# Optimization experiments

Measured on AMD Instinct MI355X. Metric: run time of the kernel, lower is better.

Reference implementation:

```python
import jax, jax.numpy as jnp
from jax import lax
import numpy as np

B, C, T, H, HEADS = 256, 16, 256, 128, 4
D = H // HEADS  # per-head graph-attention out_features = 32

def _ln(x, g, b, eps=1e-5):
    m = x.mean(-1, keepdims=True)
    v = ((x - m) ** 2).mean(-1, keepdims=True)
    return (x - m) / jnp.sqrt(v + eps) * g + b

def _gat(h_in, W, a_src, a_dst, adj):
    # GAT-style multi-head attention over channels with learnable additive adjacency mask
    n, c, _ = h_in.shape
    h = (h_in @ W).reshape(n, c, HEADS, D)
    es = jnp.einsum('nchd,hd->nch', h, a_src)
    ed = jnp.einsum('nchd,hd->nch', h, a_dst)
    e = jax.nn.leaky_relu(es[:, :, None, :] + ed[:, None, :, :], 0.2) + adj[None, :, :, None]
    a = jax.nn.softmax(e, axis=2)
    return jnp.einsum('nijh,njhd->nihd', a, h).reshape(n, c, HEADS * D)

def _lstm_dir(xseq, Wih, Whh, bih, bhh, reverse):
    b = xseq.shape[0]
    h0 = jnp.zeros((b, H), xseq.dtype)
    def step(carry, xt):
        hp, cp = carry
        g = xt @ Wih.T + hp @ Whh.T + bih + bhh
        i, f, gg, o = jnp.split(g, 4, axis=-1)  # torch gate order i,f,g,o
        cn = jax.nn.sigmoid(f) * cp + jax.nn.sigmoid(i) * jnp.tanh(gg)
        hn = jax.nn.sigmoid(o) * jnp.tanh(cn)
        return (hn, cn), hn
    _, hs = lax.scan(step, (h0, h0), jnp.swapaxes(xseq, 0, 1), reverse=reverse)
    return jnp.swapaxes(hs, 0, 1)

def setup_inputs():
    key = jax.random.key(0)
    ks = iter(jax.random.split(key, 80))
    def rn(shape, s=0.05):
        return jax.random.normal(next(ks), shape, jnp.float32) * s
    inp = {'x': jax.random.normal(next(ks), (B, C, T), jnp.float32)}
    inp.update(conv1_w=rn((32, 1, 7), 0.2), conv1_b=jnp.zeros((32,)), bn1_g=jnp.ones((32,)), bn1_b=jnp.zeros((32,)),
               conv2_w=rn((64, 32, 5), 0.1), conv2_b=jnp.zeros((64,)), bn2_g=jnp.ones((64,)), bn2_b=jnp.zeros((64,)))
    inp.update(g1_W=rn((64, H)), g1_asrc=rn((HEADS, D)), g1_adst=rn((HEADS, D)), g1_adj=rn((C, C)),
               n1_g=jnp.ones((H,)), n1_b=jnp.zeros((H,)),
               g2_W=rn((H, H)), g2_asrc=rn((HEADS, D)), g2_adst=rn((HEADS, D)), g2_adj=rn((C, C)),
               n2_g=jnp.ones((H,)), n2_b=jnp.zeros((H,)))
    for layer, din in ((0, H * C), (1, 2 * H)):
        for d in ('f', 'r'):
            inp['l%d%s_Wih' % (layer, d)] = rn((4 * H, din))
            inp['l%d%s_Whh' % (layer, d)] = rn((4 * H, H))
            inp['l%d%s_bih' % (layer, d)] = jnp.zeros((4 * H,))
            inp['l%d%s_bhh' % (layer, d)] = jnp.zeros((4 * H,))
    E = 2 * H
    inp.update(mha_wqkv=rn((3 * E, E)), mha_bqkv=jnp.zeros((3 * E,)), mha_wo=rn((E, E)), mha_bo=jnp.zeros((E,)),
               an_g=jnp.ones((E,)), an_b=jnp.zeros((E,)), pn_g=jnp.ones((2 * E,)), pn_b=jnp.zeros((2 * E,)),
               fc1_w=rn((H, 2 * E)), fc1_b=jnp.zeros((H,)), fc2_w=rn((1, H)), fc2_b=jnp.zeros((1,)))
    return inp

def reference(x, conv1_w, conv1_b, bn1_g, bn1_b, conv2_w, conv2_b, bn2_g, bn2_b,
              g1_W, g1_asrc, g1_adst, g1_adj, n1_g, n1_b,
              g2_W, g2_asrc, g2_adst, g2_adj, n2_g, n2_b,
              l0f_Wih, l0f_Whh, l0f_bih, l0f_bhh, l0r_Wih, l0r_Whh, l0r_bih, l0r_bhh,
              l1f_Wih, l1f_Whh, l1f_bih, l1f_bhh, l1r_Wih, l1r_Whh, l1r_bih, l1r_bhh,
              mha_wqkv, mha_bqkv, mha_wo, mha_bo, an_g, an_b, pn_g, pn_b,
              fc1_w, fc1_b, fc2_w, fc2_b):
    b, c, t = x.shape
    dn = ('NCH', 'OIH', 'NCH')
    # shared per-channel temporal conv: fold channels into batch (same math as the python loop)
    h = lax.conv_general_dilated(x.reshape(b * c, 1, t), conv1_w, (1,), [(3, 3)], dimension_numbers=dn) + conv1_b[None, :, None]
    h = jax.nn.gelu(h * bn1_g[None, :, None] + bn1_b[None, :, None], approximate=False)  # BN in eval mode
    h = lax.conv_general_dilated(h, conv2_w, (2,), [(2, 2)], dimension_numbers=dn) + conv2_b[None, :, None]
    h = jax.nn.gelu(h * bn2_g[None, :, None] + bn2_b[None, :, None], approximate=False)
    tc = h.shape[-1]  # 128
    # fold timesteps into batch: graph attention applied independently per t
    g = h.reshape(b, c, 64, tc).transpose(0, 3, 1, 2).reshape(b * tc, c, 64)
    g = _ln(jax.nn.relu(_gat(g, g1_W, g1_asrc, g1_adst, g1_adj)), n1_g, n1_b)
    g = _ln(jax.nn.relu(_gat(g, g2_W, g2_asrc, g2_adst, g2_adj)), n2_g, n2_b)
    seq = g.reshape(b, tc, c * H)  # (B, 128, 2048)
    o = jnp.concatenate([_lstm_dir(seq, l0f_Wih, l0f_Whh, l0f_bih, l0f_bhh, False),
                         _lstm_dir(seq, l0r_Wih, l0r_Whh, l0r_bih, l0r_bhh, True)], -1)
    o = jnp.concatenate([_lstm_dir(o, l1f_Wih, l1f_Whh, l1f_bih, l1f_bhh, False),
                         _lstm_dir(o, l1r_Wih, l1r_Whh, l1r_bih, l1r_bhh, True)], -1)
    e = o.shape[-1]
    hd = e // HEADS
    qkv = o @ mha_wqkv.T + mha_bqkv
    q, k, v = [z.reshape(b, tc, HEADS, hd).transpose(0, 2, 1, 3) for z in jnp.split(qkv, 3, axis=-1)]
    a = jax.nn.softmax(jnp.einsum('bhqd,bhkd->bhqk', q, k) * (hd ** -0.5), axis=-1)
    ao = jnp.einsum('bhqk,bhkd->bhqd', a, v).transpose(0, 2, 1, 3).reshape(b, tc, e) @ mha_wo.T + mha_bo
    att = _ln(ao + o, an_g, an_b)
    pooled = _ln(jnp.concatenate([att.mean(axis=1), att.max(axis=1)], axis=-1), pn_g, pn_b)
    return jax.nn.relu(pooled @ fc1_w.T + fc1_b) @ fc2_w.T + fc2_b
```

## Files before the change

### kernel.cpp

```cpp
#include <hip/hip_runtime.h>
#include <hip/hip_bf16.h>
#include <stdint.h>


typedef __attribute__((ext_vector_type(8))) short bh8;
typedef __attribute__((ext_vector_type(4))) float f32x4;

__device__ __forceinline__ float bfu2f(unsigned short u) {
  union { unsigned u; float f; } x; x.u = ((unsigned)u) << 16; return x.f;
}
__device__ __forceinline__ unsigned short f2bfu(float f) {
  __hip_bfloat16 h = __float2bfloat16(f);
  return *reinterpret_cast<unsigned short*>(&h);
}
__device__ __forceinline__ float geluf(float v) {
  return 0.5f * v * (1.f + erff(v * 0.70710678118f));
}
__device__ __forceinline__ float sigmoidf_(float x) { return 1.f / (1.f + __expf(-x)); }
__device__ __forceinline__ float tanh_(float x) {
  x = fminf(fmaxf(x, -30.f), 30.f);
  float e = __expf(2.f * x);
  return (e - 1.f) / (e + 1.f);
}

__device__ __forceinline__ void g2l16(const void* g, void* l) {
  __builtin_amdgcn_global_load_lds(
      (const __attribute__((address_space(1))) unsigned int*)g,
      (__attribute__((address_space(3))) unsigned int*)l, 16, 0, 0);
}

__global__ __launch_bounds__(256) void cvt_bf16_k(const float* __restrict__ s,
                                                  __hip_bfloat16* __restrict__ d, int n) {
  int i = blockIdx.x * 256 + threadIdx.x;
  if (i < n) d[i] = __float2bfloat16(s[i]);
}

__global__ __launch_bounds__(256)
void gat_waug_k(const float* __restrict__ W, const float* __restrict__ asrc,
                const float* __restrict__ adst, __hip_bfloat16* __restrict__ waug,
                int K) {
  int idx = blockIdx.x * 256 + threadIdx.x;
  if (idx >= 144 * K) return;
  const int row = idx / K, k = idx % K;
  float v = 0.f;
  if (row < 128) {
    v = W[k * 128 + row];
  } else if (row < 136) {
    const int h = (row - 128) & 3;
    const float* av = (row < 132) ? asrc : adst;
    for (int d = 0; d < 32; d++) v += W[k * 128 + h * 32 + d] * av[h * 32 + d];
  }
  waug[row * K + k] = __float2bfloat16(v);
}

__global__ __launch_bounds__(256)
void conv1_k(const float* __restrict__ x, const float* __restrict__ w,
             const float* __restrict__ b, const float* __restrict__ g,
             const float* __restrict__ bb, __hip_bfloat16* __restrict__ c1) {
  __shared__ float xs[264];
  const int nn = blockIdx.x, t = threadIdx.x;
  xs[3 + t] = x[nn * 256 + t];
  if (t < 3) { xs[t] = 0.f; xs[259 + t] = 0.f; }
  __syncthreads();
  for (int oc = 0; oc < 32; oc++) {
    float acc = 0.f;
#pragma unroll
    for (int k = 0; k < 7; k++) acc += xs[t + k] * w[oc * 7 + k];
    float v = (acc + b[oc]) * g[oc] + bb[oc];
    c1[(nn * 32 + oc) * 256 + t] = __float2bfloat16(geluf(v));
  }
}

__global__ __launch_bounds__(256)
void conv2_k(const __hip_bfloat16* __restrict__ c1, const float* __restrict__ w2,
             const float* __restrict__ b2, const float* __restrict__ g2,
             const float* __restrict__ bb2, __hip_bfloat16* __restrict__ g0) {
  __shared__ float ins[32 * 264];
  __shared__ float wsh[64 * 161];
  const int nn = blockIdx.x, tid = threadIdx.x;
  for (int idx = tid; idx < 64 * 160; idx += 256)
    wsh[(idx / 160) * 161 + idx % 160] = w2[idx];
  for (int idx = tid; idx < 32 * 4; idx += 256) {
    int ic = idx >> 2, p = idx & 3;
    ins[ic * 264 + (p < 2 ? p : 256 + p)] = 0.f;
  }
  for (int idx = tid; idx < 32 * 256; idx += 256) {
    int ic = idx >> 8, xq = idx & 255;
    ins[ic * 264 + 2 + xq] = __bfloat162float(c1[(nn * 32 + ic) * 256 + xq]);
  }
  __syncthreads();
  const int oc = tid & 63, tq = tid >> 6;
  float acc[32];
#pragma unroll
  for (int jj = 0; jj < 32; jj++) acc[jj] = 0.f;
  for (int ic = 0; ic < 32; ic++) {
    float wk0 = wsh[oc * 161 + ic * 5 + 0], wk1 = wsh[oc * 161 + ic * 5 + 1];
    float wk2 = wsh[oc * 161 + ic * 5 + 2], wk3 = wsh[oc * 161 + ic * 5 + 3];
    float wk4 = wsh[oc * 161 + ic * 5 + 4];
    const float* row = &ins[ic * 264];
#pragma unroll
    for (int jj = 0; jj < 32; jj++) {
      const int xb = tq * 64 + 2 * jj;
      acc[jj] += row[xb] * wk0 + row[xb + 1] * wk1 + row[xb + 2] * wk2 +
                 row[xb + 3] * wk3 + row[xb + 4] * wk4;
    }
  }
  const int b = nn >> 4, c = nn & 15;
  const float gg = g2[oc], bbv = bb2[oc], bs = b2[oc];
#pragma unroll
  for (int jj = 0; jj < 32; jj++) {
    const int to = tq * 32 + jj;
    float v = (acc[jj] + bs) * gg + bbv;
    g0[((long)(b * 128 + to) * 16 + c) * 64 + oc] = __float2bfloat16(geluf(v));
  }
}

template <bool OUT_BF16>
__global__ __launch_bounds__(256)
void gemm_bt(const __hip_bfloat16* __restrict__ A, const __hip_bfloat16* __restrict__ Bm,
             void* __restrict__ Cout, const float* __restrict__ bias,
             int M, int N, int K) {
  __shared__ __align__(16) __hip_bfloat16 sA[128 * 32];
  __shared__ __align__(16) __hip_bfloat16 sB[128 * 32];
  const int tid = threadIdx.x;
  const int lane = tid & 63, wv = tid >> 6;
  const int wr = wv >> 1, wc = wv & 1;
  const long m0 = (long)blockIdx.y * 128;
  const long n0 = (long)blockIdx.x * 128;
  const int sa0 = wv * 128 + lane, sa1 = wv * 128 + 64 + lane;
  const int ra0 = sa0 >> 2, ca0 = sa0 & 3;
  const int ra1 = sa1 >> 2, ca1 = sa1 & 3;
  const __hip_bfloat16* a0 = A + (m0 + ra0) * K + ca0 * 8;
  const __hip_bfloat16* a1 = A + (m0 + ra1) * K + ca1 * 8;
  const __hip_bfloat16* b0 = Bm + (n0 + ra0) * K + ca0 * 8;
  const __hip_bfloat16* b1 = Bm + (n0 + ra1) * K + ca1 * 8;
  char* lA0 = (char*)sA + wv * 2048;
  char* lA1 = (char*)sA + wv * 2048 + 1024;
  char* lB0 = (char*)sB + wv * 2048;
  char* lB1 = (char*)sB + wv * 2048 + 1024;
  f32x4 acc[4][4] = {};
  const int rfA = wr * 64 + (lane & 15);
  const int rfB = wc * 64 + (lane & 15);
  const int kf = (lane >> 4) * 8;
  for (int kt = 0; kt < K; kt += 32) {
    __syncthreads();
    g2l16(a0 + kt, lA0);
    g2l16(a1 + kt, lA1);
    g2l16(b0 + kt, lB0);
    g2l16(b1 + kt, lB1);
    __syncthreads();
    bh8 af[4], bf[4];
#pragma unroll
    for (int m = 0; m < 4; m++) af[m] = *(const bh8*)(sA + (rfA + m * 16) * 32 + kf);
#pragma unroll
    for (int n = 0; n < 4; n++) bf[n] = *(const bh8*)(sB + (rfB + n * 16) * 32 + kf);
#pragma unroll
    for (int m = 0; m < 4; m++)
#pragma unroll
      for (int n = 0; n < 4; n++)
        acc[m][n] = __builtin_amdgcn_mfma_f32_16x16x32_bf16(af[m], bf[n], acc[m][n], 0, 0, 0);
  }
#pragma unroll
  for (int n = 0; n < 4; n++) {
    const long col = n0 + wc * 64 + n * 16 + (lane & 15);
    const float bv = bias ? bias[col] : 0.f;
#pragma unroll
    for (int m = 0; m < 4; m++) {
      const long row0 = m0 + wr * 64 + m * 16 + ((lane >> 4) * 4);
#pragma unroll
      for (int r = 0; r < 4; r++) {
        float v = acc[m][n][r] + bv;
        if (OUT_BF16)
          ((__hip_bfloat16*)Cout)[(row0 + r) * N + col] = __float2bfloat16(v);
        else
          ((float*)Cout)[(row0 + r) * N + col] = v;
      }
    }
  }
}

template <int K>
__global__ __launch_bounds__(128)
void gat_fused_k(const __hip_bfloat16* __restrict__ hin,
                 const __hip_bfloat16* __restrict__ waug,
                 const float* __restrict__ adj, const float* __restrict__ lng,
                 const float* __restrict__ lnb, __hip_bfloat16* __restrict__ outp) {
  const long n = blockIdx.x;
  const int f = threadIdx.x;
  const int lane = f & 63, wv = f >> 6;
  const int head = f >> 5;
  __shared__ float hs[16][132];
  __shared__ float adj_s[16][16];
  __shared__ float es_s[16][4], ed_s[16][4];
  __shared__ float a_s[16][65];
  __shared__ float mean_s[16], rs_s[16];
  const __hip_bfloat16* An = hin + n * 16 * K;
  const int ar = lane & 15, hi = lane >> 4, ak = hi * 8;
  f32x4 pacc[4] = {};
  f32x4 pe = {};
  for (int kt = 0; kt < K; kt += 32) {
    const bh8 af = *(const bh8*)(An + ar * K + kt + ak);
#pragma unroll
    for (int s = 0; s < 4; s++) {
      const bh8 bf = *(const bh8*)(waug + (wv * 64 + s * 16 + ar) * K + kt + ak);
      pacc[s] = __builtin_amdgcn_mfma_f32_16x16x32_bf16(af, bf, pacc[s], 0, 0, 0);
    }
    if (wv == 0) {
      const bh8 be = *(const bh8*)(waug + (128 + ar) * K + kt + ak);
      pe = __builtin_amdgcn_mfma_f32_16x16x32_bf16(af, be, pe, 0, 0, 0);
    }
  }
  for (int idx = f; idx < 256; idx += 128) adj_s[idx >> 4][idx & 15] = adj[idx];
#pragma unroll
  for (int s = 0; s < 4; s++)
#pragma unroll
    for (int r = 0; r < 4; r++)
      hs[hi * 4 + r][wv * 64 + s * 16 + ar] = pacc[s][r];
  if (wv == 0 && ar < 8) {
#pragma unroll
    for (int r = 0; r < 4; r++) {
      const int c = hi * 4 + r;
      if (ar < 4) es_s[c][ar] = pe[r];
      else        ed_s[c][ar - 4] = pe[r];
    }
  }
  __syncthreads();
  if (f < 64) {
    const int i = f >> 2, hd = f & 3;
    float ev[16], mx = -1e30f;
#pragma unroll
    for (int j = 0; j < 16; j++) {
      float e = es_s[i][hd] + ed_s[j][hd];
      e = (e > 0.f ? e : 0.2f * e) + adj_s[i][j];
      ev[j] = e; mx = fmaxf(mx, e);
    }
    float sm = 0.f;
#pragma unroll
    for (int j = 0; j < 16; j++) { ev[j] = __expf(ev[j] - mx); sm += ev[j]; }
    const float inv = 1.f / sm;
#pragma unroll
    for (int j = 0; j < 16; j++) a_s[i][j * 4 + hd] = ev[j] * inv;
  }
  __syncthreads();
  float hv[16];
#pragma unroll
  for (int c = 0; c < 16; c++) hv[c] = hs[c][f];
  __syncthreads();
  float o[16];
#pragma unroll
  for (int i = 0; i < 16; i++) {
    float acc = 0.f;
#pragma unroll
    for (int j = 0; j < 16; j++) acc += a_s[i][j * 4 + head] * hv[j];
    acc = fmaxf(acc, 0.f);
    o[i] = acc;
    hs[i][f] = acc;
  }
  __syncthreads();
  {
    const int i = f >> 3, g = f & 7;
    float s = 0.f, ss = 0.f;
#pragma unroll
    for (int q = 0; q < 16; q++) {
      const float v = hs[i][g * 16 + q];
      s += v; ss += v * v;
    }
#pragma unroll
    for (int m = 1; m < 8; m <<= 1) { s += __shfl_xor(s, m); ss += __shfl_xor(ss, m); }
    if (g == 0) {
      const float mean = s * (1.f / 128.f);
      const float var = ss * (1.f / 128.f) - mean * mean;
      mean_s[i] = mean;
      rs_s[i] = rsqrtf(var + 1e-5f);
    }
  }
  __syncthreads();
  const float gw = lng[f], gb = lnb[f];
#pragma unroll
  for (int i = 0; i < 16; i++)
    outp[(n * 16 + i) * 128 + f] = __float2bfloat16((o[i] - mean_s[i]) * rs_s[i] * gw + gb);
}

__global__ __launch_bounds__(512)
void lstm_mfma_k(const float* __restrict__ gates, const float* __restrict__ whh,
                 const float* __restrict__ bih, const float* __restrict__ bhh,
                 __hip_bfloat16* __restrict__ outp, const int dir, const int colOff) {
  const int chunk = blockIdx.x;
  const int tid = threadIdx.x;
  const int lane = tid & 63, w = tid >> 6;
  const int cl = lane & 15, hi = lane >> 4;
  __shared__ __align__(16) __hip_bfloat16 h_frag[2048];
  __shared__ float g_lds[2][520];
  for (int idx = tid; idx < 1024; idx += 512) ((unsigned*)h_frag)[idx] = 0u;
  bh8 bfr[4][4];
#pragma unroll
  for (int n = 0; n < 4; n++)
#pragma unroll
    for (int kt = 0; kt < 4; kt++) {
      const float* wp = whh + (w * 64 + n * 16 + cl) * 128 + kt * 32 + hi * 8;
      const float4 lo = *(const float4*)wp;
      const float4 hv = *(const float4*)(wp + 4);
      bh8 r;
      r[0] = (short)f2bfu(lo.x); r[1] = (short)f2bfu(lo.y);
      r[2] = (short)f2bfu(lo.z); r[3] = (short)f2bfu(lo.w);
      r[4] = (short)f2bfu(hv.x); r[5] = (short)f2bfu(hv.y);
      r[6] = (short)f2bfu(hv.z); r[7] = (short)f2bfu(hv.w);
      bfr[n][kt] = r;
    }
  float bs[4];
#pragma unroll
  for (int n = 0; n < 4; n++)
    bs[n] = bih[w * 64 + n * 16 + cl] + bhh[w * 64 + n * 16 + cl];
  const int ub = tid >> 7, uj = tid & 127;
  float c_st = 0.f;
  __syncthreads();
  for (int s = 0; s < 128; s++) {
    const int t = dir ? (127 - s) : s;
    float gin[4][2];
    if (hi == 0) {
#pragma unroll
      for (int n = 0; n < 4; n++)
#pragma unroll
        for (int r = 0; r < 2; r++)
          gin[n][r] = gates[((long)(chunk * 2 + r) * 128 + t) * 512 + w * 64 + n * 16 + cl];
    }
    bh8 af[4];
#pragma unroll
    for (int kt = 0; kt < 4; kt++)
      af[kt] = *(const bh8*)(h_frag + kt * 512 + lane * 8);
    f32x4 acc[4] = {};
#pragma unroll
    for (int n = 0; n < 4; n++)
#pragma unroll
      for (int kt = 0; kt < 4; kt++)
        acc[n] = __builtin_amdgcn_mfma_f32_16x16x32_bf16(af[kt], bfr[n][kt], acc[n], 0, 0, 0);
    if (hi == 0) {
#pragma unroll
      for (int n = 0; n < 4; n++)
#pragma unroll
        for (int r = 0; r < 2; r++)
          g_lds[r][w * 64 + n * 16 + cl] = acc[n][r] + gin[n][r] + bs[n];
    }
    __syncthreads();
    if (tid < 256) {
      const float gi = sigmoidf_(g_lds[ub][uj]);
      const float gf = sigmoidf_(g_lds[ub][uj + 128]);
      const float gg = tanh_(g_lds[ub][uj + 256]);
      const float go = sigmoidf_(g_lds[ub][uj + 384]);
      const float c = gf * c_st + gi * gg;
      c_st = c;
      const float hh = go * tanh_(c);
      h_frag[(uj >> 5) * 512 + ((uj >> 3) & 3) * 128 + ub * 8 + (uj & 7)] =
          __float2bfloat16(hh);
      outp[((long)(chunk * 2 + ub) * 128 + t) * 256 + colOff + uj] = __float2bfloat16(hh);
    }
    __syncthreads();
  }
}

#define DOT8T(Q, O, KV)                                                        \
  (Q[(O) + 0] * bfu2f((unsigned short)(KV)[0]) +                               \
   Q[(O) + 1] * bfu2f((unsigned short)(KV)[1]) +                               \
   Q[(O) + 2] * bfu2f((unsigned short)(KV)[2]) +                               \
   Q[(O) + 3] * bfu2f((unsigned short)(KV)[3]) +                               \
   Q[(O) + 4] * bfu2f((unsigned short)(KV)[4]) +                               \
   Q[(O) + 5] * bfu2f((unsigned short)(KV)[5]) +                               \
   Q[(O) + 6] * bfu2f((unsigned short)(KV)[6]) +                               \
   Q[(O) + 7] * bfu2f((unsigned short)(KV)[7]))

__global__ __launch_bounds__(256)
void mha_k(const __hip_bfloat16* __restrict__ qkv, __hip_bfloat16* __restrict__ ao) {
  const int bh = blockIdx.x;
  const int b = bh >> 2, hd = bh & 3;
  const int tid = threadIdx.x;
  __shared__ __align__(16) __hip_bfloat16 ks[128 * 68];
  __shared__ __align__(16) __hip_bfloat16 vs[128 * 68];
  __shared__ __align__(16) char xreg[33792];
  __shared__ float mx_s[2][128], sm_s[2][128];
  const long base = (long)b * 128 * 768 + hd * 64;
  for (int idx = tid; idx < 3072; idx += 256) {
    const int mm = idx >> 10, cc = idx & 1023;
    const int t = cc >> 3, c8 = cc & 7;
    const bh8 val = *(const bh8*)(qkv + base + (long)t * 768 + mm * 256 + c8 * 8);
    __hip_bfloat16* dst = (mm == 0) ? (__hip_bfloat16*)xreg : (mm == 1 ? ks : vs);
    *(bh8*)(dst + t * 68 + c8 * 8) = val;
  }
  __syncthreads();
  const int i = tid & 127;
  const int jh = tid >> 7;
  float qf[64];
#pragma unroll
  for (int kk = 0; kk < 8; kk++) {
    const bh8 v8 = *(const bh8*)((const __hip_bfloat16*)xreg + i * 68 + kk * 8);
#pragma unroll
    for (int e = 0; e < 8; e++) qf[kk * 8 + e] = bfu2f((unsigned short)v8[e]);
  }
  float s[64];
#pragma unroll
  for (int jo = 0; jo < 64; jo++) {
    const int j = jh * 64 + jo;
    float acc = 0.f;
#pragma unroll
    for (int kk = 0; kk < 8; kk++) {
      const bh8 kv = *(const bh8*)(ks + j * 68 + kk * 8);
      acc += DOT8T(qf, kk * 8, kv);
    }
    s[jo] = acc * 0.125f;
  }
  float mx = -1e30f;
#pragma unroll
  for (int jo = 0; jo < 64; jo++) mx = fmaxf(mx, s[jo]);
  mx_s[jh][i] = mx;
  __syncthreads();
  const float m = fmaxf(mx_s[0][i], mx_s[1][i]);
  float sum = 0.f;
#pragma unroll
  for (int jo = 0; jo < 64; jo++) { s[jo] = __expf(s[jo] - m); sum += s[jo]; }
  sm_s[jh][i] = sum;
  __syncthreads();
  const float inv = 1.f / (sm_s[0][i] + sm_s[1][i]);
  __hip_bfloat16* P = (__hip_bfloat16*)xreg;
#pragma unroll
  for (int jo = 0; jo < 64; jo += 2) {
    const unsigned u = (unsigned)f2bfu(s[jo] * inv) | ((unsigned)f2bfu(s[jo + 1] * inv) << 16);
    *(unsigned*)(P + i * 132 + jh * 64 + jo) = u;
  }
  __syncthreads();
  const int dh = jh;
  float acc[32];
#pragma unroll
  for (int e = 0; e < 32; e++) acc[e] = 0.f;
  for (int j = 0; j < 128; j++) {
    const float p = bfu2f(*(const unsigned short*)(P + i * 132 + j));
#pragma unroll
    for (int kk = 0; kk < 4; kk++) {
      const bh8 vv = *(const bh8*)(vs + j * 68 + dh * 32 + kk * 8);
      acc[kk * 8 + 0] += p * bfu2f((unsigned short)vv[0]);
      acc[kk * 8 + 1] += p * bfu2f((unsigned short)vv[1]);
      acc[kk * 8 + 2] += p * bfu2f((unsigned short)vv[2]);
      acc[kk * 8 + 3] += p * bfu2f((unsigned short)vv[3]);
      acc[kk * 8 + 4] += p * bfu2f((unsigned short)vv[4]);
      acc[kk * 8 + 5] += p * bfu2f((unsigned short)vv[5]);
      acc[kk * 8 + 6] += p * bfu2f((unsigned short)vv[6]);
      acc[kk * 8 + 7] += p * bfu2f((unsigned short)vv[7]);
    }
  }
  const long ob = ((long)b * 128 + i) * 256 + hd * 64 + dh * 32;
#pragma unroll
  for (int kk = 0; kk < 16; kk++) {
    const unsigned u = (unsigned)f2bfu(acc[2 * kk]) | ((unsigned)f2bfu(acc[2 * kk + 1]) << 16);
    *(unsigned*)(ao + ob + kk * 2) = u;
  }
}

__global__ __launch_bounds__(256)
void resid_ln_k(const float* __restrict__ proj, const __hip_bfloat16* __restrict__ o,
                const float* __restrict__ g, const float* __restrict__ bb,
                float* __restrict__ att) {
  const long m = blockIdx.x;
  const int t = threadIdx.x;
  const float v = proj[m * 256 + t] + __bfloat162float(o[m * 256 + t]);
  float sv = v, ssv = v * v;
#pragma unroll
  for (int mm = 1; mm < 64; mm <<= 1) { sv += __shfl_xor(sv, mm); ssv += __shfl_xor(ssv, mm); }
  __shared__ float red[4][2];
  const int lane = t & 63, wv = t >> 6;
  if (lane == 0) { red[wv][0] = sv; red[wv][1] = ssv; }
  __syncthreads();
  const float S = red[0][0] + red[1][0] + red[2][0] + red[3][0];
  const float SS = red[0][1] + red[1][1] + red[2][1] + red[3][1];
  const float mu = S * (1.f / 256.f);
  const float rr = rsqrtf(SS * (1.f / 256.f) - mu * mu + 1e-5f);
  att[m * 256 + t] = (v - mu) * rr * g[t] + bb[t];
}

__global__ __launch_bounds__(256)
void pool_k(const float* __restrict__ att, const float* __restrict__ png,
            const float* __restrict__ pnb, const float* __restrict__ f1w,
            const float* __restrict__ f1b, const float* __restrict__ f2w,
            const float* __restrict__ f2b, float* __restrict__ outp) {
  const int b = blockIdx.x, e = threadIdx.x;
  float sum = 0.f, mx = -1e30f;
  for (int t = 0; t < 128; t++) {
    const float v = att[((long)b * 128 + t) * 256 + e];
    sum += v; mx = fmaxf(mx, v);
  }
  const float a0 = sum * (1.f / 128.f), a1 = mx;
  float sv = a0 + a1, ssv = a0 * a0 + a1 * a1;
#pragma unroll
  for (int mm = 1; mm < 64; mm <<= 1) { sv += __shfl_xor(sv, mm); ssv += __shfl_xor(ssv, mm); }
  __shared__ float red[4][2];
  __shared__ float y[512];
  __shared__ float z[128];
  const int lane = e & 63, wv = e >> 6;
  if (lane == 0) { red[wv][0] = sv; red[wv][1] = ssv; }
  __syncthreads();
  const float S = red[0][0] + red[1][0] + red[2][0] + red[3][0];
  const float SS = red[0][1] + red[1][1] + red[2][1] + red[3][1];
  const float mu = S * (1.f / 512.f);
  const float rr = rsqrtf(SS * (1.f / 512.f) - mu * mu + 1e-5f);
  y[e] = (a0 - mu) * rr * png[e] + pnb[e];
  y[256 + e] = (a1 - mu) * rr * png[256 + e] + pnb[256 + e];
  __syncthreads();
  if (e < 128) {
    float a = f1b[e];
    for (int k = 0; k < 512; k++) a += y[k] * f1w[e * 512 + k];
    z[e] = fmaxf(a, 0.f);
  }
  __syncthreads();
  if (e < 64) {
    float p = z[e] * f2w[e] + z[e + 64] * f2w[e + 64];
#pragma unroll
    for (int mm = 1; mm < 64; mm <<= 1) p += __shfl_xor(p, mm);
    if (e == 0) outp[b] = p + f2b[0];
  }
}

extern "C" void kernel_launch(void* const* d_in, const int* in_sizes, int n_in,
                              void* d_out, int out_size, void* d_ws, size_t ws_size,
                              hipStream_t stream) {
  (void)in_sizes; (void)n_in; (void)out_size; (void)ws_size;
  const float* x      = (const float*)d_in[0];
  const float* c1w    = (const float*)d_in[1];
  const float* c1b    = (const float*)d_in[2];
  const float* bn1g   = (const float*)d_in[3];
  const float* bn1b   = (const float*)d_in[4];
  const float* c2w    = (const float*)d_in[5];
  const float* c2b    = (const float*)d_in[6];
  const float* bn2g   = (const float*)d_in[7];
  const float* bn2b   = (const float*)d_in[8];
  const float* g1W    = (const float*)d_in[9];
  const float* g1asrc = (const float*)d_in[10];
  const float* g1adst = (const float*)d_in[11];
  const float* g1adj  = (const float*)d_in[12];
  const float* n1g    = (const float*)d_in[13];
  const float* n1b    = (const float*)d_in[14];
  const float* g2W    = (const float*)d_in[15];
  const float* g2asrc = (const float*)d_in[16];
  const float* g2adst = (const float*)d_in[17];
  const float* g2adj  = (const float*)d_in[18];
  const float* n2g    = (const float*)d_in[19];
  const float* n2b    = (const float*)d_in[20];
  const float* l0fWih = (const float*)d_in[21];
  const float* l0fWhh = (const float*)d_in[22];
  const float* l0fbih = (const float*)d_in[23];
  const float* l0fbhh = (const float*)d_in[24];
  const float* l0rWih = (const float*)d_in[25];
  const float* l0rWhh = (const float*)d_in[26];
  const float* l0rbih = (const float*)d_in[27];
  const float* l0rbhh = (const float*)d_in[28];
  const float* l1fWih = (const float*)d_in[29];
  const float* l1fWhh = (const float*)d_in[30];
  const float* l1fbih = (const float*)d_in[31];
  const float* l1fbhh = (const float*)d_in[32];
  const float* l1rWih = (const float*)d_in[33];
  const float* l1rWhh = (const float*)d_in[34];
  const float* l1rbih = (const float*)d_in[35];
  const float* l1rbhh = (const float*)d_in[36];
  const float* wqkv   = (const float*)d_in[37];
  const float* bqkv   = (const float*)d_in[38];
  const float* wo     = (const float*)d_in[39];
  const float* bo     = (const float*)d_in[40];
  const float* ang    = (const float*)d_in[41];
  const float* anb    = (const float*)d_in[42];
  const float* png    = (const float*)d_in[43];
  const float* pnb    = (const float*)d_in[44];
  const float* f1w    = (const float*)d_in[45];
  const float* f1b    = (const float*)d_in[46];
  const float* f2w    = (const float*)d_in[47];
  const float* f2b    = (const float*)d_in[48];

  char* ws = (char*)d_ws;
  auto G0   = (__hip_bfloat16*)(ws + 0L);
  auto C1   = (__hip_bfloat16*)(ws + 67108864L);
  auto G1O  = (__hip_bfloat16*)(ws + 67108864L);
  auto GAF  = (float*)(ws + 0L);
  auto OUT0 = (__hip_bfloat16*)(ws + 201326592L);
  auto OUT1 = (__hip_bfloat16*)(ws + 67108864L);
  auto QKV  = (__hip_bfloat16*)(ws + 83886080L);
  auto AOb  = (__hip_bfloat16*)(ws + 134217728L);
  auto PROJ = (float*)(ws + 150994944L);
  auto ATT  = (float*)(ws + 184549376L);
  auto WAUG1 = (__hip_bfloat16*)(ws + 201326592L);
  auto WAUG2 = (__hip_bfloat16*)(ws + 201326592L + 20480L);
  char* WB  = ws + 218103808L;
  auto WI0F  = (__hip_bfloat16*)(WB + 49152);
  auto WI0R  = (__hip_bfloat16*)(WB + 2146304);
  auto WI1F  = (__hip_bfloat16*)(WB + 4243456);
  auto WI1R  = (__hip_bfloat16*)(WB + 4505600);
  auto WQKVb = (__hip_bfloat16*)(WB + 4767744);
  auto WOb   = (__hip_bfloat16*)(WB + 5160960);

  gat_waug_k<<<36, 256, 0, stream>>>(g1W, g1asrc, g1adst, WAUG1, 64);
  gat_waug_k<<<72, 256, 0, stream>>>(g2W, g2asrc, g2adst, WAUG2, 128);
  cvt_bf16_k<<<4096, 256, 0, stream>>>(l0fWih, WI0F, 1048576);
  cvt_bf16_k<<<4096, 256, 0, stream>>>(l0rWih, WI0R, 1048576);
  cvt_bf16_k<<<512, 256, 0, stream>>>(l1fWih, WI1F, 131072);
  cvt_bf16_k<<<512, 256, 0, stream>>>(l1rWih, WI1R, 131072);
  cvt_bf16_k<<<768, 256, 0, stream>>>(wqkv, WQKVb, 196608);
  cvt_bf16_k<<<256, 256, 0, stream>>>(wo, WOb, 65536);

  conv1_k<<<4096, 256, 0, stream>>>(x, c1w, c1b, bn1g, bn1b, C1);
  conv2_k<<<4096, 256, 0, stream>>>(C1, c2w, c2b, bn2g, bn2b, G0);
  gat_fused_k<64><<<32768, 128, 0, stream>>>(G0, WAUG1, g1adj, n1g, n1b, G1O);
  gat_fused_k<128><<<32768, 128, 0, stream>>>(G1O, WAUG2, g2adj, n2g, n2b, G1O);
  gemm_bt<false><<<dim3(4, 256), 256, 0, stream>>>(G1O, WI0F, GAF, nullptr, 32768, 512, 2048);
  lstm_mfma_k<<<128, 512, 0, stream>>>(GAF, l0fWhh, l0fbih, l0fbhh, OUT0, 0, 0);
  gemm_bt<false><<<dim3(4, 256), 256, 0, stream>>>(G1O, WI0R, GAF, nullptr, 32768, 512, 2048);
  lstm_mfma_k<<<128, 512, 0, stream>>>(GAF, l0rWhh, l0rbih, l0rbhh, OUT0, 1, 128);
  gemm_bt<false><<<dim3(4, 256), 256, 0, stream>>>(OUT0, WI1F, GAF, nullptr, 32768, 512, 256);
  lstm_mfma_k<<<128, 512, 0, stream>>>(GAF, l1fWhh, l1fbih, l1fbhh, OUT1, 0, 0);
  gemm_bt<false><<<dim3(4, 256), 256, 0, stream>>>(OUT0, WI1R, GAF, nullptr, 32768, 512, 256);
  lstm_mfma_k<<<128, 512, 0, stream>>>(GAF, l1rWhh, l1rbih, l1rbhh, OUT1, 1, 128);
  gemm_bt<true><<<dim3(6, 256), 256, 0, stream>>>(OUT1, WQKVb, QKV, bqkv, 32768, 768, 256);
  mha_k<<<1024, 256, 0, stream>>>(QKV, AOb);
  gemm_bt<false><<<dim3(2, 256), 256, 0, stream>>>(AOb, WOb, PROJ, bo, 32768, 256, 256);
  resid_ln_k<<<32768, 256, 0, stream>>>(PROJ, OUT1, ang, anb, ATT);
  pool_k<<<256, 256, 0, stream>>>(ATT, png, pnb, f1w, f1b, f2w, f2b, (float*)d_out);
}
```

Before: 1.706 ms.

## Run conv2 as implicit GEMM on MFMA and remap GEMM tiles across XCDs

Replaces the scalar FP32 conv2 with an implicit-GEMM kernel on bf16 MFMA. The input is staged in LDS in a swizzled (column, channel) layout, and the weights are pre-packed per tap by a small prep kernel that also folds bias and BN into a scale and shift. Separately, the GEMM kernel remaps its block index so that consecutive tiles land on the same XCD, which aims to improve L2 reuse. The conv2 rewrite removes large FP32 LDS staging and scalar FMA work, at the cost of a bf16 accumulation-input path and an extra prep launch.

Result: faster. 1.448 ms (-15.1%).

```diff
diff --git a/kernel.cpp b/kernel.cpp
--- a/kernel.cpp
+++ b/kernel.cpp
@@ -54,6 +54,20 @@
 }
 
 __global__ __launch_bounds__(256)
+void conv2w_k(const float* __restrict__ w2, const float* __restrict__ b2,
+              const float* __restrict__ g2, const float* __restrict__ bb2,
+              __hip_bfloat16* __restrict__ wc2, float* __restrict__ sc,
+              float* __restrict__ sh) {
+  const int tid = blockIdx.x * 256 + threadIdx.x;
+  if (tid < 64 * 160) {
+    const int oc = tid / 160, k = tid % 160;
+    const int kt = k >> 5, ic = k & 31;
+    wc2[tid] = __float2bfloat16(w2[oc * 160 + ic * 5 + kt]);
+  }
+  if (tid < 64) { sc[tid] = g2[tid]; sh[tid] = b2[tid] * g2[tid] + bb2[tid]; }
+}
+
+__global__ __launch_bounds__(256)
 void conv1_k(const float* __restrict__ x, const float* __restrict__ w,
              const float* __restrict__ b, const float* __restrict__ g,
              const float* __restrict__ bb, __hip_bfloat16* __restrict__ c1) {
@@ -72,46 +86,73 @@
 }
 
 __global__ __launch_bounds__(256)
-void conv2_k(const __hip_bfloat16* __restrict__ c1, const float* __restrict__ w2,
-             const float* __restrict__ b2, const float* __restrict__ g2,
-             const float* __restrict__ bb2, __hip_bfloat16* __restrict__ g0) {
-  __shared__ float ins[32 * 264];
-  __shared__ float wsh[64 * 161];
+void conv2_mfma_k(const __hip_bfloat16* __restrict__ c1,
+                  const __hip_bfloat16* __restrict__ wc2,
+                  const float* __restrict__ scale, const float* __restrict__ shift,
+                  __hip_bfloat16* __restrict__ g0) {
   const int nn = blockIdx.x, tid = threadIdx.x;
-  for (int idx = tid; idx < 64 * 160; idx += 256)
-    wsh[(idx / 160) * 161 + idx % 160] = w2[idx];
-  for (int idx = tid; idx < 32 * 4; idx += 256) {
-    int ic = idx >> 2, p = idx & 3;
-    ins[ic * 264 + (p < 2 ? p : 256 + p)] = 0.f;
-  }
-  for (int idx = tid; idx < 32 * 256; idx += 256) {
-    int ic = idx >> 8, xq = idx & 255;
-    ins[ic * 264 + 2 + xq] = __bfloat162float(c1[(nn * 32 + ic) * 256 + xq]);
-  }
-  __syncthreads();
-  const int oc = tid & 63, tq = tid >> 6;
-  float acc[32];
-#pragma unroll
-  for (int jj = 0; jj < 32; jj++) acc[jj] = 0.f;
-  for (int ic = 0; ic < 32; ic++) {
-    float wk0 = wsh[oc * 161 + ic * 5 + 0], wk1 = wsh[oc * 161 + ic * 5 + 1];
-    float wk2 = wsh[oc * 161 + ic * 5 + 2], wk3 = wsh[oc * 161 + ic * 5 + 3];
-    float wk4 = wsh[oc * 161 + ic * 5 + 4];
-    const float* row = &ins[ic * 264];
-#pragma unroll
-    for (int jj = 0; jj < 32; jj++) {
-      const int xb = tq * 64 + 2 * jj;
-      acc[jj] += row[xb] * wk0 + row[xb + 1] * wk1 + row[xb + 2] * wk2 +
-                 row[xb + 3] * wk3 + row[xb + 4] * wk4;
+  const int lane = tid & 63, wv = tid >> 6;
+  const int cl = lane & 15, hi = lane >> 4;
+  __shared__ __align__(16) __hip_bfloat16 L[260 * 32];
+  __shared__ float sc_s[64], sh_s[64];
+  if (tid < 64) {
+    const int pcol = (tid >> 4) < 2 ? (tid >> 4) : 256 + (tid >> 4);
+    ((unsigned*)L)[pcol * 16 + (tid & 15)] = 0u;
+  }
+  if (tid >= 64 && tid < 128) { sc_s[tid - 64] = scale[tid - 64]; sh_s[tid - 64] = shift[tid - 64]; }
+  {
+    const int ic2 = tid & 15, tg = tid >> 4;
+    const __hip_bfloat16* r0 = c1 + ((long)nn * 32 + 2 * ic2) * 256 + tg * 16;
+    const bh8 v0a = *(const bh8*)(r0);
+    const bh8 v0b = *(const bh8*)(r0 + 8);
+    const bh8 v1a = *(const bh8*)(r0 + 256);
+    const bh8 v1b = *(const bh8*)(r0 + 264);
+    const int g = ic2 >> 2;
+#pragma unroll
+    for (int e = 0; e < 16; e++) {
+      const int col = tg * 16 + e + 2;
+      const unsigned lo = (unsigned)(unsigned short)((e < 8) ? v0a[e] : v0b[e - 8]);
+      const unsigned hh = (unsigned)(unsigned short)((e < 8) ? v1a[e] : v1b[e - 8]);
+      const int pos = (g ^ ((col >> 1) & 3)) * 8 + ((2 * ic2) & 7);
+      *(unsigned*)((char*)L + col * 64 + pos * 2) = lo | (hh << 16);
+    }
+  }
+  bh8 af[4][5];
+#pragma unroll
+  for (int mt = 0; mt < 4; mt++)
+#pragma unroll
+    for (int kt = 0; kt < 5; kt++)
+      af[mt][kt] = *(const bh8*)(wc2 + (mt * 16 + cl) * 160 + kt * 32 + hi * 8);
+  __syncthreads();
+  f32x4 acc[4][2] = {};
+#pragma unroll
+  for (int nf = 0; nf < 2; nf++) {
+    const int to = wv * 32 + nf * 16 + cl;
+#pragma unroll
+    for (int kt = 0; kt < 5; kt++) {
+      const int col = 2 * to + kt;
+      const bh8 bf = *(const bh8*)((const char*)L + col * 64 + ((hi ^ ((col >> 1) & 3)) * 8) * 2);
+#pragma unroll
+      for (int mt = 0; mt < 4; mt++)
+        acc[mt][nf] = __builtin_amdgcn_mfma_f32_16x16x32_bf16(af[mt][kt], bf, acc[mt][nf], 0, 0, 0);
     }
   }
   const int b = nn >> 4, c = nn & 15;
-  const float gg = g2[oc], bbv = bb2[oc], bs = b2[oc];
-#pragma unroll
-  for (int jj = 0; jj < 32; jj++) {
-    const int to = tq * 32 + jj;
-    float v = (acc[jj] + bs) * gg + bbv;
-    g0[((long)(b * 128 + to) * 16 + c) * 64 + oc] = __float2bfloat16(geluf(v));
+#pragma unroll
+  for (int nf = 0; nf < 2; nf++) {
+    const int to = wv * 32 + nf * 16 + cl;
+    __hip_bfloat16* outb = g0 + ((long)(b * 128 + to) * 16 + c) * 64;
+#pragma unroll
+    for (int mt = 0; mt < 4; mt++) {
+      ushort4 pk;
+      unsigned short* pp = (unsigned short*)&pk;
+#pragma unroll
+      for (int r = 0; r < 4; r++) {
+        const int oc = mt * 16 + hi * 4 + r;
+        pp[r] = f2bfu(geluf(acc[mt][nf][r] * sc_s[oc] + sh_s[oc]));
+      }
+      *(ushort4*)(outb + mt * 16 + hi * 4) = pk;
+    }
   }
 }
 
@@ -125,8 +166,15 @@
   const int tid = threadIdx.x;
   const int lane = tid & 63, wv = tid >> 6;
   const int wr = wv >> 1, wc = wv & 1;
-  const long m0 = (long)blockIdx.y * 128;
-  const long n0 = (long)blockIdx.x * 128;
+  int fid = blockIdx.y * gridDim.x + blockIdx.x;
+  {
+    const int nwg = gridDim.x * gridDim.y;
+    const int q = nwg >> 3, r = nwg & 7;
+    const int xcd = fid & 7, off = fid >> 3;
+    fid = (xcd < r ? xcd * (q + 1) : r * (q + 1) + (xcd - r) * q) + off;
+  }
+  const long m0 = (long)(fid / gridDim.x) * 128;
+  const long n0 = (long)(fid % gridDim.x) * 128;
   const int sa0 = wv * 128 + lane, sa1 = wv * 128 + 64 + lane;
   const int ra0 = sa0 >> 2, ca0 = sa0 & 3;
   const int ra1 = sa1 >> 2, ca1 = sa1 & 3;
@@ -584,6 +632,9 @@
   auto WAUG1 = (__hip_bfloat16*)(ws + 201326592L);
   auto WAUG2 = (__hip_bfloat16*)(ws + 201326592L + 20480L);
   char* WB  = ws + 218103808L;
+  auto WC2   = (__hip_bfloat16*)(WB + 0);
+  auto SC2   = (float*)(WB + 20480);
+  auto SH2   = (float*)(WB + 20736);
   auto WI0F  = (__hip_bfloat16*)(WB + 49152);
   auto WI0R  = (__hip_bfloat16*)(WB + 2146304);
   auto WI1F  = (__hip_bfloat16*)(WB + 4243456);
@@ -593,6 +644,7 @@
 
   gat_waug_k<<<36, 256, 0, stream>>>(g1W, g1asrc, g1adst, WAUG1, 64);
   gat_waug_k<<<72, 256, 0, stream>>>(g2W, g2asrc, g2adst, WAUG2, 128);
+  conv2w_k<<<40, 256, 0, stream>>>(c2w, c2b, bn2g, bn2b, WC2, SC2, SH2);
   cvt_bf16_k<<<4096, 256, 0, stream>>>(l0fWih, WI0F, 1048576);
   cvt_bf16_k<<<4096, 256, 0, stream>>>(l0rWih, WI0R, 1048576);
   cvt_bf16_k<<<512, 256, 0, stream>>>(l1fWih, WI1F, 131072);
@@ -601,7 +653,7 @@
   cvt_bf16_k<<<256, 256, 0, stream>>>(wo, WOb, 65536);
 
   conv1_k<<<4096, 256, 0, stream>>>(x, c1w, c1b, bn1g, bn1b, C1);
-  conv2_k<<<4096, 256, 0, stream>>>(C1, c2w, c2b, bn2g, bn2b, G0);
+  conv2_mfma_k<<<4096, 256, 0, stream>>>(C1, WC2, SC2, SH2, G0);
   gat_fused_k<64><<<32768, 128, 0, stream>>>(G0, WAUG1, g1adj, n1g, n1b, G1O);
   gat_fused_k<128><<<32768, 128, 0, stream>>>(G1O, WAUG2, g2adj, n2g, n2b, G1O);
   gemm_bt<false><<<dim3(4, 256), 256, 0, stream>>>(G1O, WI0F, GAF, nullptr, 32768, 512, 2048);
```
